# Kernel optimization log

Measured on AMD Instinct MI355X. Metric: run time of the kernel, lower is better.

The kernel has to match this reference:

```python
import jax, jax.numpy as jnp
import numpy as np
from jax import lax

R = 4                 # radius (init kwarg)
EPS = 2.0             # eps (init kwarg)
K = 2 * R + 1         # stencil size


def _dir_kernels():
    """8 directional box kernels [8,1,K,K]: L,R,U,D,NW,NE,SW,SE (matches torch construction)."""
    base = np.ones((K, K), np.float32)
    L = base.copy(); L[:, R + 1:] = 0
    Rk = base.copy(); Rk[:, :R] = 0
    U = base.copy(); U[R + 1:, :] = 0
    D = base.copy(); D[:R, :] = 0
    NW = U.copy(); NE = U.copy(); SW = D.copy(); SE = D.copy()
    half = float((R + 1) * (2 * R + 1))
    L, Rk, U, D = L / half, Rk / half, U / half, D / half
    NW[:, R + 1:] = 0; NE[:, :R] = 0; SW[:, R + 1:] = 0; SE[:, :R] = 0
    quad = float((R + 1) ** 2)
    NW, NE, SW, SE = NW / quad, NE / quad, SW / quad, SE / quad
    return jnp.asarray(np.stack([L, Rk, U, D, NW, NE, SW, SE])[:, None])


def _pad(x):
    # ReplicationPad2d(R)
    return jnp.pad(x, ((0, 0), (0, 0), (R, R), (R, R)), mode='edge')


def _conv(x, w, groups=1):
    return lax.conv_general_dilated(
        x, w, window_strides=(1, 1), padding='VALID',
        dimension_numbers=('NCHW', 'OIHW', 'NCHW'), feature_group_count=groups)


def _resize_bilinear_ac(x, H, W):
    """Bilinear resize with align_corners=True, separable gather. x: [N,C,h,w]."""
    n, c, h, w = x.shape
    dt = x.dtype

    def coords(out, src):
        t = jnp.arange(out, dtype=dt) * (jnp.asarray(src - 1, dt) / jnp.asarray(out - 1, dt))
        i0 = jnp.clip(jnp.floor(t).astype(jnp.int32), 0, src - 2)
        f = t - i0.astype(dt)
        return i0, f

    y0, fy = coords(H, h)
    x0, fx = coords(W, w)
    rows = x[:, :, y0, :] * (1 - fy)[None, None, :, None] + x[:, :, y0 + 1, :] * fy[None, None, :, None]
    return rows[:, :, :, x0] * (1 - fx) + rows[:, :, :, x0 + 1] * fx


def setup_inputs() -> dict:
    key = jax.random.key(0)
    k1, k2, k3 = jax.random.split(key, 3)
    lr_x = jax.random.uniform(k1, (1, 3, 256, 256), jnp.float32) * 255.0
    lr_y = jax.random.uniform(k2, (1, 3, 256, 256), jnp.float32) * 255.0
    hr_x = jax.random.uniform(k3, (1, 3, 1024, 1024), jnp.float32) * 255.0
    box_w = jnp.full((3, 1, K, K), 1.0 / (K * K), jnp.float32)  # depthwise box filter weights
    return {"lr_x": lr_x, "lr_y": lr_y, "hr_x": hr_x, "box_w": box_w}


def reference(lr_x, lr_y, hr_x, box_w):
    H, W = hr_x.shape[2], hr_x.shape[3]
    box = lambda t: _conv(_pad(t), box_w, groups=3)

    # --- guided filter coefficients at low res ---
    mean_x = box(lr_x)
    mean_y = box(lr_y)
    cov_xy = box(lr_x * lr_y) - mean_x * mean_y
    var_x = box(lr_x * lr_x) - mean_x * mean_x
    A = cov_xy / (var_x + EPS)
    b = mean_y - A * mean_x

    # --- upsample A, b to hr (bilinear, align_corners=True) ---
    A = _resize_bilinear_ac(A, H, W)
    b = _resize_bilinear_ac(b, H, W)

    # --- 8-direction side-window stencil; channels treated as batch ---
    dirw = _dir_kernels()                      # [8,1,K,K]
    A3 = _pad(A.reshape(3, 1, H, W))
    b3 = _pad(b.reshape(3, 1, H, W))
    im3 = hr_x.reshape(3, 1, H, W)
    cA = _conv(A3, dirw)                       # [3,8,H,W]
    cB = _conv(b3, dirw)                       # [3,8,H,W]
    d = cA * im3 + cB - im3                    # [3,8,H,W]

    idx = jnp.argmin(jnp.abs(d), axis=1, keepdims=True)
    dm = jnp.take_along_axis(d, idx, axis=1)   # min-|delta| direction
    res = (dm + im3).reshape(1, 3, H, W)

    # res.int() truncates toward zero, then clamp(0,255), then float
    return jnp.clip(jnp.trunc(res), 0.0, 255.0)
```

## Files before the change

### kernel.cpp

```cpp
#include <hip/hip_runtime.h>

#define RR 4
#define LRN 256
#define HRN 1024
#define SCALE (255.0f/1023.0f)

typedef float v2 __attribute__((ext_vector_type(2)));

#define WS_LUTW 4096
#define WS_AB   65536

__device__ inline int anchor_of(int u) {
    int k = min(max(u - 4, 0), HRN - 1);
    float t = (float)k * SCALE;
    int i = (int)t; if (i > LRN - 2) i = LRN - 2;
    return i;
}

__device__ inline float4 mkw(int k0, int k1, int a) {
    float4 w = make_float4(0.f, 0.f, 0.f, 0.f);
    for (int k = k0; k <= k1; ++k) {
        int kc = min(max(k, 0), HRN - 1);
        float t = (float)kc * SCALE;
        int i = (int)t; if (i > LRN - 2) i = LRN - 2;
        float f = t - (float)i;
        int off = i - a;
        float wa = 1.0f - f, wb = f;
        w.x += (off == 0) ? wa : 0.0f;
        w.y += (off == 1) ? wa : ((off == 0) ? wb : 0.0f);
        w.z += (off == 2) ? wa : ((off == 1) ? wb : 0.0f);
        w.w += (off == 2) ? wb : 0.0f;
    }
    return w;
}

__global__ __launch_bounds__(256, 4) void lr_kernel(
    const float* __restrict__ lrx, const float* __restrict__ lry,
    float* __restrict__ ws)
{
    __shared__ float4 sV[24][40];
    __shared__ float4 sHS[24][32];

    const int c  = blockIdx.z;
    const int X0 = blockIdx.x * 32, Y0 = blockIdx.y * 16;
    const int tid = threadIdx.y * 32 + threadIdx.x;
    const float* px = lrx + c * LRN * LRN;
    const float* py = lry + c * LRN * LRN;

    if (c == 0 && blockIdx.y == 0 && tid < 128) {
        int u = blockIdx.x * 128 + tid;
        int a = anchor_of(u);
        ((int*)ws)[u] = a;
        float4* w = (float4*)((char*)ws + WS_LUTW) + u * 3;
        w[0] = mkw(u - 4, u,     a);
        w[1] = mkw(u,     u + 4, a);
        w[2] = mkw(u - 4, u + 4, a);
    }

    for (int i = tid; i < 24 * 40; i += 256) {
        int r = i / 40, cc = i - r * 40;
        int gy = min(max(Y0 - 4 + r, 0), LRN - 1);
        int gx = min(max(X0 - 4 + cc, 0), LRN - 1);
        float xv = px[gy * LRN + gx];
        float yv = py[gy * LRN + gx];
        sV[r][cc] = make_float4(xv, yv, xv * yv, xv * xv);
    }
    __syncthreads();

    for (int i = tid; i < 24 * 32; i += 256) {
        int r = i / 32, cc = i & 31;
        float4 s = sV[r][cc];
        #pragma unroll
        for (int k = 1; k < 9; ++k) {
            float4 v = sV[r][cc + k];
            s.x += v.x; s.y += v.y; s.z += v.z; s.w += v.w;
        }
        sHS[r][cc] = s;
    }
    __syncthreads();

    v2* ab_out = (v2*)((char*)ws + WS_AB);
    for (int i = tid; i < 16 * 32; i += 256) {
        int r = i / 32, cc = i & 31;
        float4 s = sHS[r][cc];
        #pragma unroll
        for (int k = 1; k < 9; ++k) {
            float4 v = sHS[r + k][cc];
            s.x += v.x; s.y += v.y; s.z += v.z; s.w += v.w;
        }
        const float inv81 = 1.0f / 81.0f;
        float mx = s.x * inv81, my = s.y * inv81;
        float cov = s.z * inv81 - mx * my;
        float var = s.w * inv81 - mx * mx;
        float A = cov / (var + 2.0f);
        float B = my - A * mx;
        v2 ab; ab.x = A; ab.y = B;
        ab_out[(c * LRN + (Y0 + r)) * LRN + X0 + cc] = ab;
    }
}

#define TX 32
#define TYR 32
#define BTH 8
#define NROW (TYR / BTH)
#define LRC 12
#define LRR 12

__global__ __launch_bounds__(256, 7) void hr_kernel(
    const float* __restrict__ hrx, const float* __restrict__ ws,
    float* __restrict__ out)
{
    __shared__ float4 sTB[TYR][LRC];
    __shared__ v2     sF[TYR][LRC];
    __shared__ v2     sAB[LRR][LRC];
    __shared__ float4 sYW[TYR][3];
    __shared__ int    sYA[TYR];
    __shared__ float4 sXW[TX][3];
    __shared__ int    sXA[TX];

    const int c  = blockIdx.z;
    const int X0 = blockIdx.x * TX, Y0 = blockIdx.y * TYR;
    const int tid = threadIdx.y * TX + threadIdx.x;

    const int*    lutA = (const int*)ws;
    const float4* lutW = (const float4*)((const char*)ws + WS_LUTW);
    const v2*     AB   = (const v2*)((const char*)ws + WS_AB) + c * LRN * LRN;

    const int rowbase = lutA[Y0];
    const int colbase = lutA[X0];

    if (tid < TX) {
        int u = X0 + tid;
        sXA[tid] = lutA[u] - colbase;
        sXW[tid][0] = lutW[u * 3 + 0];
        sXW[tid][1] = lutW[u * 3 + 1];
        sXW[tid][2] = lutW[u * 3 + 2];
    } else if (tid >= 64 && tid < 64 + TYR) {
        int r = tid - 64, u = Y0 + r;
        sYA[r] = lutA[u] - rowbase;
        sYW[r][0] = lutW[u * 3 + 0];
        sYW[r][1] = lutW[u * 3 + 1];
        sYW[r][2] = lutW[u * 3 + 2];
    } else if (tid >= 96 && tid < 96 + LRR * LRC) {
        int i = tid - 96;
        int r = i / LRC, cc = i - r * LRC;
        int gy = min(rowbase + r, LRN - 1);
        int gx = min(colbase + cc, LRN - 1);
        sAB[r][cc] = AB[gy * LRN + gx];
    }
    __syncthreads();

    for (int i = tid; i < TYR * LRC; i += 256) {
        int r = i / LRC, cc = i - r * LRC;
        int ra = sYA[r];
        float4 wT = sYW[r][0], wB = sYW[r][1], wF = sYW[r][2];
        v2 v0 = sAB[ra][cc],     v1 = sAB[ra + 1][cc];
        v2 v2_ = sAB[ra + 2][cc], v3 = sAB[ra + 3][cc];
        v2 t, b, f;
        t = v0 * wT.x; t = __builtin_elementwise_fma((v2)(wT.y), v1, t);
        t = __builtin_elementwise_fma((v2)(wT.z), v2_, t);
        t = __builtin_elementwise_fma((v2)(wT.w), v3, t);
        b = v0 * wB.x; b = __builtin_elementwise_fma((v2)(wB.y), v1, b);
        b = __builtin_elementwise_fma((v2)(wB.z), v2_, b);
        b = __builtin_elementwise_fma((v2)(wB.w), v3, b);
        f = v0 * wF.x; f = __builtin_elementwise_fma((v2)(wF.y), v1, f);
        f = __builtin_elementwise_fma((v2)(wF.z), v2_, f);
        f = __builtin_elementwise_fma((v2)(wF.w), v3, f);
        sTB[r][cc] = make_float4(t.x, t.y, b.x, b.y);
        sF[r][cc]  = f;
    }
    __syncthreads();

    const int tx = threadIdx.x, tyw = threadIdx.y;
    const int c0 = sXA[tx];
    const float4 wL = sXW[tx][0], wR = sXW[tx][1], wFh = sXW[tx][2];
    const float i45 = 1.0f / 45.0f, i25 = 1.0f / 25.0f;
    const float* hp = hrx + (c * HRN + Y0 + tyw) * HRN + X0 + tx;
    float*       op = out + (c * HRN + Y0 + tyw) * HRN + X0 + tx;

    #pragma unroll
    for (int j = 0; j < NROW; ++j) {
        const int r = tyw + j * BTH;
        v2 aL = 0, aR = 0, aU = 0, aD = 0;
        v2 aNW = 0, aNE = 0, aSW = 0, aSE = 0;
        #pragma unroll
        for (int k = 0; k < 4; ++k) {
            float wl = (k==0)?wL.x:(k==1)?wL.y:(k==2)?wL.z:wL.w;
            float wr = (k==0)?wR.x:(k==1)?wR.y:(k==2)?wR.z:wR.w;
            float wf = (k==0)?wFh.x:(k==1)?wFh.y:(k==2)?wFh.z:wFh.w;
            float4 tb = sTB[r][c0 + k];
            v2 tv; tv.x = tb.x; tv.y = tb.y;
            v2 bv; bv.x = tb.z; bv.y = tb.w;
            v2 fv = sF[r][c0 + k];
            aL  = __builtin_elementwise_fma((v2)(wl), fv, aL);
            aR  = __builtin_elementwise_fma((v2)(wr), fv, aR);
            aU  = __builtin_elementwise_fma((v2)(wf), tv, aU);
            aD  = __builtin_elementwise_fma((v2)(wf), bv, aD);
            aNW = __builtin_elementwise_fma((v2)(wl), tv, aNW);
            aNE = __builtin_elementwise_fma((v2)(wr), tv, aNE);
            aSW = __builtin_elementwise_fma((v2)(wl), bv, aSW);
            aSE = __builtin_elementwise_fma((v2)(wr), bv, aSE);
        }
        float xv = hp[j * BTH * HRN];

        float d0 = fmaf(i45, fmaf(aL.x,  xv, aL.y),  -xv);
        float d1 = fmaf(i45, fmaf(aR.x,  xv, aR.y),  -xv);
        float d2 = fmaf(i45, fmaf(aU.x,  xv, aU.y),  -xv);
        float d3 = fmaf(i45, fmaf(aD.x,  xv, aD.y),  -xv);
        float d4 = fmaf(i25, fmaf(aNW.x, xv, aNW.y), -xv);
        float d5 = fmaf(i25, fmaf(aNE.x, xv, aNE.y), -xv);
        float d6 = fmaf(i25, fmaf(aSW.x, xv, aSW.y), -xv);
        float d7 = fmaf(i25, fmaf(aSE.x, xv, aSE.y), -xv);

        float a0 = fabsf(d0), a1 = fabsf(d1), a2 = fabsf(d2), a3 = fabsf(d3);
        float a4 = fabsf(d4), a5 = fabsf(d5), a6 = fabsf(d6), a7 = fabsf(d7);
        bool c01 = a0 <= a1; float w01 = c01 ? d0 : d1; float m01 = c01 ? a0 : a1;
        bool c23 = a2 <= a3; float w23 = c23 ? d2 : d3; float m23 = c23 ? a2 : a3;
        bool c45 = a4 <= a5; float w45 = c45 ? d4 : d5; float m45 = c45 ? a4 : a5;
        bool c67 = a6 <= a7; float w67 = c67 ? d6 : d7; float m67 = c67 ? a6 : a7;
        bool cA_ = m01 <= m23; float wA = cA_ ? w01 : w23; float mA = cA_ ? m01 : m23;
        bool cB_ = m45 <= m67; float wB_ = cB_ ? w45 : w67; float mB = cB_ ? m45 : m67;
        float bd = (mA <= mB) ? wA : wB_;

        float res = __builtin_amdgcn_fmed3f(truncf(bd + xv), 0.0f, 255.0f);
        op[j * BTH * HRN] = res;
    }
}

extern "C" void kernel_launch(void* const* d_in, const int* in_sizes, int n_in,
                              void* d_out, int out_size, void* d_ws, size_t ws_size,
                              hipStream_t stream) {
    const float* lrx = (const float*)d_in[0];
    const float* lry = (const float*)d_in[1];
    const float* hrx = (const float*)d_in[2];
    (void)d_in[3]; (void)in_sizes; (void)n_in; (void)out_size; (void)ws_size;

    float* ws   = (float*)d_ws;
    float* outp = (float*)d_out;

    lr_kernel<<<dim3(LRN / 32, LRN / 16, 3), dim3(32, 8), 0, stream>>>(lrx, lry, ws);
    hr_kernel<<<dim3(HRN / TX, HRN / TYR, 3), dim3(TX, BTH), 0, stream>>>(hrx, ws, outp);
}
```

Measured before the change: 85.35 us.

## Swap separable pass order: horizontal prepass in shared, vertical sliding window in registers

The hr kernel now does the horizontal (column) interpolation-weighted prepass over the low-res rows into shared memory, then each thread walks 8 consecutive output rows and keeps a 4-row register window that shifts only when the low-res anchor row changes. Tiles grow to 64x32 with 64x4 threads, which cuts the shared-memory reads per output pixel and the redundant prepass work across tiles. In exchange each thread keeps more live registers, the occupancy hint drops to 6 blocks, and the per-row window-shift branch may diverge.

```diff
diff --git a/kernel.cpp b/kernel.cpp
--- a/kernel.cpp
+++ b/kernel.cpp
@@ -1,6 +1,5 @@
 #include <hip/hip_runtime.h>
 
-#define RR 4
 #define LRN 256
 #define HRN 1024
 #define SCALE (255.0f/1023.0f)
@@ -99,27 +98,27 @@
     }
 }
 
-#define TX 32
-#define TYR 32
-#define BTH 8
-#define NROW (TYR / BTH)
-#define LRC 12
+#define TX 64
+#define TYV 32
+#define WROWS 8
+#define LRC 20
 #define LRR 12
 
-__global__ __launch_bounds__(256, 7) void hr_kernel(
+__global__ __launch_bounds__(256, 6) void hr_kernel(
     const float* __restrict__ hrx, const float* __restrict__ ws,
     float* __restrict__ out)
 {
-    __shared__ float4 sTB[TYR][LRC];
-    __shared__ v2     sF[TYR][LRC];
+    __shared__ v2     sHL[LRR][TX];
+    __shared__ v2     sHR[LRR][TX];
+    __shared__ v2     sHF[LRR][TX];
     __shared__ v2     sAB[LRR][LRC];
-    __shared__ float4 sYW[TYR][3];
-    __shared__ int    sYA[TYR];
     __shared__ float4 sXW[TX][3];
     __shared__ int    sXA[TX];
+    __shared__ float4 sYW[TYV][3];
+    __shared__ int    sYA[TYV];
 
     const int c  = blockIdx.z;
-    const int X0 = blockIdx.x * TX, Y0 = blockIdx.y * TYR;
+    const int X0 = blockIdx.x * TX, Y0 = blockIdx.y * TYV;
     const int tid = threadIdx.y * TX + threadIdx.x;
 
     const int*    lutA = (const int*)ws;
@@ -135,14 +134,14 @@
         sXW[tid][0] = lutW[u * 3 + 0];
         sXW[tid][1] = lutW[u * 3 + 1];
         sXW[tid][2] = lutW[u * 3 + 2];
-    } else if (tid >= 64 && tid < 64 + TYR) {
-        int r = tid - 64, u = Y0 + r;
+    } else if (tid < TX + TYV) {
+        int r = tid - TX, u = Y0 + r;
         sYA[r] = lutA[u] - rowbase;
         sYW[r][0] = lutW[u * 3 + 0];
         sYW[r][1] = lutW[u * 3 + 1];
         sYW[r][2] = lutW[u * 3 + 2];
-    } else if (tid >= 96 && tid < 96 + LRR * LRC) {
-        int i = tid - 96;
+    }
+    for (int i = tid; i < LRR * LRC; i += 256) {
         int r = i / LRC, cc = i - r * LRC;
         int gy = min(rowbase + r, LRN - 1);
         int gx = min(colbase + cc, LRN - 1);
@@ -150,58 +149,73 @@
     }
     __syncthreads();
 
-    for (int i = tid; i < TYR * LRC; i += 256) {
-        int r = i / LRC, cc = i - r * LRC;
-        int ra = sYA[r];
-        float4 wT = sYW[r][0], wB = sYW[r][1], wF = sYW[r][2];
-        v2 v0 = sAB[ra][cc],     v1 = sAB[ra + 1][cc];
-        v2 v2_ = sAB[ra + 2][cc], v3 = sAB[ra + 3][cc];
-        v2 t, b, f;
-        t = v0 * wT.x; t = __builtin_elementwise_fma((v2)(wT.y), v1, t);
-        t = __builtin_elementwise_fma((v2)(wT.z), v2_, t);
-        t = __builtin_elementwise_fma((v2)(wT.w), v3, t);
-        b = v0 * wB.x; b = __builtin_elementwise_fma((v2)(wB.y), v1, b);
-        b = __builtin_elementwise_fma((v2)(wB.z), v2_, b);
-        b = __builtin_elementwise_fma((v2)(wB.w), v3, b);
-        f = v0 * wF.x; f = __builtin_elementwise_fma((v2)(wF.y), v1, f);
-        f = __builtin_elementwise_fma((v2)(wF.z), v2_, f);
-        f = __builtin_elementwise_fma((v2)(wF.w), v3, f);
-        sTB[r][cc] = make_float4(t.x, t.y, b.x, b.y);
-        sF[r][cc]  = f;
+    for (int i = tid; i < LRR * TX; i += 256) {
+        int r = i >> 6, x = i & 63;
+        int c0 = sXA[x];
+        float4 wL = sXW[x][0], wR = sXW[x][1], wF = sXW[x][2];
+        v2 a0 = sAB[r][c0],     a1 = sAB[r][c0 + 1];
+        v2 a2 = sAB[r][c0 + 2], a3 = sAB[r][c0 + 3];
+        v2 hl, hr_, hf;
+        hl  = a0 * wL.x;
+        hl  = __builtin_elementwise_fma((v2)(wL.y), a1, hl);
+        hl  = __builtin_elementwise_fma((v2)(wL.z), a2, hl);
+        hl  = __builtin_elementwise_fma((v2)(wL.w), a3, hl);
+        hr_ = a0 * wR.x;
+        hr_ = __builtin_elementwise_fma((v2)(wR.y), a1, hr_);
+        hr_ = __builtin_elementwise_fma((v2)(wR.z), a2, hr_);
+        hr_ = __builtin_elementwise_fma((v2)(wR.w), a3, hr_);
+        hf  = a0 * wF.x;
+        hf  = __builtin_elementwise_fma((v2)(wF.y), a1, hf);
+        hf  = __builtin_elementwise_fma((v2)(wF.z), a2, hf);
+        hf  = __builtin_elementwise_fma((v2)(wF.w), a3, hf);
+        sHL[r][x] = hl; sHR[r][x] = hr_; sHF[r][x] = hf;
     }
     __syncthreads();
 
     const int tx = threadIdx.x, tyw = threadIdx.y;
-    const int c0 = sXA[tx];
-    const float4 wL = sXW[tx][0], wR = sXW[tx][1], wFh = sXW[tx][2];
+    const int row0 = tyw * WROWS;
     const float i45 = 1.0f / 45.0f, i25 = 1.0f / 25.0f;
-    const float* hp = hrx + (c * HRN + Y0 + tyw) * HRN + X0 + tx;
-    float*       op = out + (c * HRN + Y0 + tyw) * HRN + X0 + tx;
+    const float* hp = hrx + (c * HRN + Y0 + row0) * HRN + X0 + tx;
+    float*       op = out + (c * HRN + Y0 + row0) * HRN + X0 + tx;
+
+    int rap = sYA[row0];
+    v2 hL0 = sHL[rap][tx],     hL1 = sHL[rap + 1][tx];
+    v2 hL2 = sHL[rap + 2][tx], hL3 = sHL[rap + 3][tx];
+    v2 hR0 = sHR[rap][tx],     hR1 = sHR[rap + 1][tx];
+    v2 hR2 = sHR[rap + 2][tx], hR3 = sHR[rap + 3][tx];
+    v2 hF0 = sHF[rap][tx],     hF1 = sHF[rap + 1][tx];
+    v2 hF2 = sHF[rap + 2][tx], hF3 = sHF[rap + 3][tx];
 
     #pragma unroll
-    for (int j = 0; j < NROW; ++j) {
-        const int r = tyw + j * BTH;
+    for (int j = 0; j < WROWS; ++j) {
+        const int yr = row0 + j;
+        const int ra = sYA[yr];
+        if (ra != rap) {
+            hL0 = hL1; hL1 = hL2; hL2 = hL3; hL3 = sHL[ra + 3][tx];
+            hR0 = hR1; hR1 = hR2; hR2 = hR3; hR3 = sHR[ra + 3][tx];
+            hF0 = hF1; hF1 = hF2; hF2 = hF3; hF3 = sHF[ra + 3][tx];
+            rap = ra;
+        }
+        const float4 wT = sYW[yr][0], wB = sYW[yr][1], wFv = sYW[yr][2];
+
         v2 aL = 0, aR = 0, aU = 0, aD = 0;
         v2 aNW = 0, aNE = 0, aSW = 0, aSE = 0;
-        #pragma unroll
-        for (int k = 0; k < 4; ++k) {
-            float wl = (k==0)?wL.x:(k==1)?wL.y:(k==2)?wL.z:wL.w;
-            float wr = (k==0)?wR.x:(k==1)?wR.y:(k==2)?wR.z:wR.w;
-            float wf = (k==0)?wFh.x:(k==1)?wFh.y:(k==2)?wFh.z:wFh.w;
-            float4 tb = sTB[r][c0 + k];
-            v2 tv; tv.x = tb.x; tv.y = tb.y;
-            v2 bv; bv.x = tb.z; bv.y = tb.w;
-            v2 fv = sF[r][c0 + k];
-            aL  = __builtin_elementwise_fma((v2)(wl), fv, aL);
-            aR  = __builtin_elementwise_fma((v2)(wr), fv, aR);
-            aU  = __builtin_elementwise_fma((v2)(wf), tv, aU);
-            aD  = __builtin_elementwise_fma((v2)(wf), bv, aD);
-            aNW = __builtin_elementwise_fma((v2)(wl), tv, aNW);
-            aNE = __builtin_elementwise_fma((v2)(wr), tv, aNE);
-            aSW = __builtin_elementwise_fma((v2)(wl), bv, aSW);
-            aSE = __builtin_elementwise_fma((v2)(wr), bv, aSE);
-        }
-        float xv = hp[j * BTH * HRN];
+        #define TAPK(WT, WB, WF, HL, HR_, HF)                         \
+            aU  = __builtin_elementwise_fma((v2)(WT), HF,  aU);       \
+            aD  = __builtin_elementwise_fma((v2)(WB), HF,  aD);       \
+            aL  = __builtin_elementwise_fma((v2)(WF), HL,  aL);       \
+            aR  = __builtin_elementwise_fma((v2)(WF), HR_, aR);       \
+            aNW = __builtin_elementwise_fma((v2)(WT), HL,  aNW);      \
+            aNE = __builtin_elementwise_fma((v2)(WT), HR_, aNE);      \
+            aSW = __builtin_elementwise_fma((v2)(WB), HL,  aSW);      \
+            aSE = __builtin_elementwise_fma((v2)(WB), HR_, aSE);
+        TAPK(wT.x, wB.x, wFv.x, hL0, hR0, hF0)
+        TAPK(wT.y, wB.y, wFv.y, hL1, hR1, hF1)
+        TAPK(wT.z, wB.z, wFv.z, hL2, hR2, hF2)
+        TAPK(wT.w, wB.w, wFv.w, hL3, hR3, hF3)
+        #undef TAPK
+
+        float xv = hp[j * HRN];
 
         float d0 = fmaf(i45, fmaf(aL.x,  xv, aL.y),  -xv);
         float d1 = fmaf(i45, fmaf(aR.x,  xv, aR.y),  -xv);
@@ -223,7 +237,7 @@
         float bd = (mA <= mB) ? wA : wB_;
 
         float res = __builtin_amdgcn_fmed3f(truncf(bd + xv), 0.0f, 255.0f);
-        op[j * BTH * HRN] = res;
+        op[j * HRN] = res;
     }
 }
 
@@ -239,5 +253,5 @@
     float* outp = (float*)d_out;
 
     lr_kernel<<<dim3(LRN / 32, LRN / 16, 3), dim3(32, 8), 0, stream>>>(lrx, lry, ws);
-    hr_kernel<<<dim3(HRN / TX, HRN / TYR, 3), dim3(TX, BTH), 0, stream>>>(hrx, ws, outp);
-}
+    hr_kernel<<<dim3(HRN / TX, HRN / TYV, 3), dim3(TX, 4), 0, stream>>>(hrx, ws, outp);
+}
```

Result: slower. 87.90 us (+3.0%).
